# Performance work log

Hardware: AMD Instinct MI355X
Metric: run time of the kernel (lower is better)

Reference implementation:

```python
import jax, jax.numpy as jnp
import numpy as np

P = 16            # decode steps == n_process
M = 4             # number of physical nodes
CAPACITY = [4, 4, 4, 4]
B = 4096          # batch
S = 16            # n_process (sequence length)
G = 128           # gnn_dim
E = 256           # n_embed
H = 512           # n_hidden
CLIP = 10.0       # clip_logits
MASK_PENALTY = 1e8


def setup_inputs() -> dict:
    key = jax.random.key(0)
    ks = jax.random.split(key, 16)
    u = lambda k, shape: jax.random.uniform(k, shape, jnp.float32, -0.08, 0.08)
    return {
        "x": jax.random.normal(ks[0], (B, S, G), jnp.float32),
        "emb_W": u(ks[1], (E, G)),                 # embedding Linear (no bias)
        "enc_Wih": u(ks[2], (4 * H, E)),           # encoder LSTM (gate order i,f,g,o)
        "enc_Whh": u(ks[3], (4 * H, H)),
        "enc_b": u(ks[4], (4 * H,)),               # b_ih + b_hh folded into one bias
        "dec_Wih": u(ks[5], (4 * H, E)),           # decoder LSTM
        "dec_Whh": u(ks[6], (4 * H, H)),
        "dec_b": u(ks[7], (4 * H,)),
        "Wq2": u(ks[8], (H, H)),                   # pointer W_q2
        "bq2": u(ks[9], (H,)),
        "Wref2": u(ks[10], (H, H)),                # pointer W_ref2 (conv1d k=1 == linear)
        "bref2": u(ks[11], (H,)),
        "Vec2": u(ks[12], (H,)),
        "dec_input0": u(ks[13], (E,)),             # learned initial decoder input
    }


def lstm_cell(x, h, c, Wih, Whh, b):
    g = x @ Wih.T + h @ Whh.T + b
    i, f, gg, o = jnp.split(g, 4, axis=-1)
    c = jax.nn.sigmoid(f) * c + jax.nn.sigmoid(i) * jnp.tanh(gg)
    h = jax.nn.sigmoid(o) * jnp.tanh(c)
    return h, c


def reference(x, emb_W, enc_Wih, enc_Whh, enc_b, dec_Wih, dec_Whh, dec_b,
              Wq2, bq2, Wref2, bref2, Vec2, dec_input0):
    Bx, Sx, _ = x.shape
    emb = x @ emb_W.T                                  # (B,S,E)

    # ---- encoder LSTM over the sequence ----
    def enc_step(carry, xt):
        h, c = carry
        h, c = lstm_cell(xt, h, c, enc_Wih, enc_Whh, enc_b)
        return (h, c), h

    h0 = jnp.zeros((Bx, H), emb.dtype)
    (h, c), enc_hs = jax.lax.scan(enc_step, (h0, h0), jnp.swapaxes(emb, 0, 1))
    ref = jnp.swapaxes(enc_hs, 0, 1)                   # (B,S,H)

    # W_ref2 conv1d(k=1) applied to ref is step-invariant: hoist out of the loop
    u2 = jnp.einsum('bsh,oh->bso', ref, Wref2) + bref2  # (B,S,H)

    dec0 = jnp.broadcast_to(dec_input0, (Bx, E))
    mask0 = jnp.zeros((Bx, Sx), emb.dtype)

    def dec_step(carry, _):
        h, c, din, mask = carry
        h, c = lstm_cell(din, h, c, dec_Wih, dec_Whh, dec_b)
        qp = h @ Wq2.T + bq2                           # (B,H)
        t = CLIP * jnp.tanh(qp[:, None, :] + u2)       # (B,S,H)
        logits = jnp.einsum('h,bsh->bs', Vec2, t) - MASK_PENALTY * mask
        log_p = jax.nn.log_softmax(logits, axis=-1)    # (B,S)
        nxt = jnp.argmax(log_p, axis=1)                # greedy node selector
        din = jnp.take_along_axis(emb, nxt[:, None, None], axis=1)[:, 0, :]
        mask = mask + jax.nn.one_hot(nxt, Sx, dtype=mask.dtype)
        return (h, c, din, mask), (nxt, log_p)

    _, (pis, log_ps) = jax.lax.scan(dec_step, (h, c, dec0, mask0), None, length=P)
    pi = jnp.swapaxes(pis, 0, 1)                       # (B,P)
    log_ps = jnp.swapaxes(log_ps, 0, 1)                # (B,P,S)

    # log-likelihood of the chosen tour
    ll = jnp.take_along_axis(log_ps, pi[:, :, None], axis=2)[..., 0].sum(axis=1)

    # __get_mapping: node id per step depends only on the capacity vector
    nodes = jnp.asarray(np.repeat(np.arange(M), np.asarray(CAPACITY))[:P], jnp.int32)
    rows = jnp.arange(Bx)
    mapping = jnp.full((Bx, P), -1, jnp.int32)
    mapping = mapping.at[rows[:, None], pi].set(jnp.broadcast_to(nodes, (Bx, P)))
    return mapping, ll
```

## Files before the change

### kernel.cpp

```cpp
#include <hip/hip_runtime.h>
#include <cstddef>

#define Bsz  4096
#define Sseq 16
#define Gdim 128
#define Edim 256
#define Hdim 512
#define H4   2048
#define Psteps 16
#define BK   16

typedef short bfrag8 __attribute__((ext_vector_type(8)));
typedef float f32x4  __attribute__((ext_vector_type(4)));

__device__ __forceinline__ void split3(float f, unsigned short& h,
                                       unsigned short& m, unsigned short& l) {
    unsigned u = __float_as_uint(f);
    h = (unsigned short)(u >> 16);
    float r1 = f - __uint_as_float(u & 0xffff0000u);
    unsigned u1 = __float_as_uint(r1);
    m = (unsigned short)(u1 >> 16);
    float r2 = r1 - __uint_as_float(u1 & 0xffff0000u);
    l = (unsigned short)(__float_as_uint(r2) >> 16);
}

__global__ void fold_kernel(const float* __restrict__ encWih,
                            const float* __restrict__ encWhh,
                            const float* __restrict__ enc_b,
                            const float* __restrict__ decWih,
                            const float* __restrict__ decWhh,
                            const float* __restrict__ dec_b,
                            const float* __restrict__ embW,
                            const float* __restrict__ dec0,
                            unsigned short* __restrict__ encEh,
                            unsigned short* __restrict__ encEm,
                            unsigned short* __restrict__ encEl,
                            unsigned short* __restrict__ encWh,
                            unsigned short* __restrict__ encWm,
                            unsigned short* __restrict__ encWl,
                            unsigned short* __restrict__ decEh,
                            unsigned short* __restrict__ decEm,
                            unsigned short* __restrict__ decEl,
                            unsigned short* __restrict__ decWh,
                            unsigned short* __restrict__ decWm,
                            unsigned short* __restrict__ decWl,
                            float* __restrict__ encBI, float* __restrict__ decBI,
                            float* __restrict__ v0bI) {
    __shared__ float rE[Edim], rD[Edim];
    const int o = blockIdx.x;
    const int gate = o >> 9, j = o & 511;
    const int c = j * 4 + gate;
    const int g = threadIdx.x;
    rE[g]        = encWih[(size_t)o * Edim + g];
    rE[g + Gdim] = encWih[(size_t)o * Edim + g + Gdim];
    rD[g]        = decWih[(size_t)o * Edim + g];
    rD[g + Gdim] = decWih[(size_t)o * Edim + g + Gdim];
    __syncthreads();

    float se = 0.f, sd = 0.f;
#pragma unroll 8
    for (int e = 0; e < Edim; ++e) {
        float w = embW[e * Gdim + g];
        se += rE[e] * w;
        sd += rD[e] * w;
    }
    unsigned short h, m, l;
    split3(se, h, m, l);
    encEh[(size_t)c * Gdim + g] = h; encEm[(size_t)c * Gdim + g] = m;
    encEl[(size_t)c * Gdim + g] = l;
    split3(sd, h, m, l);
    decEh[(size_t)c * Gdim + g] = h; decEm[(size_t)c * Gdim + g] = m;
    decEl[(size_t)c * Gdim + g] = l;
    for (int k = g; k < Hdim; k += Gdim) {
        split3(encWhh[(size_t)o * Hdim + k], h, m, l);
        encWh[(size_t)c * Hdim + k] = h; encWm[(size_t)c * Hdim + k] = m;
        encWl[(size_t)c * Hdim + k] = l;
        split3(decWhh[(size_t)o * Hdim + k], h, m, l);
        decWh[(size_t)c * Hdim + k] = h; decWm[(size_t)c * Hdim + k] = m;
        decWl[(size_t)c * Hdim + k] = l;
    }
    if (g == 0) {
        encBI[c] = enc_b[o];
        decBI[c] = dec_b[o];
        float s = dec_b[o];
        for (int e = 0; e < Edim; ++e) s += rD[e] * dec0[e];
        v0bI[c] = s;
    }
}

__global__ __launch_bounds__(256) void fold_proj(
    const float* __restrict__ Wr, const float* __restrict__ Wq,
    unsigned short* __restrict__ rWh, unsigned short* __restrict__ rWm,
    unsigned short* __restrict__ rWl,
    unsigned short* __restrict__ qWh, unsigned short* __restrict__ qWm,
    unsigned short* __restrict__ qWl) {
    const int o = blockIdx.x;
    const float* src = blockIdx.y ? Wq : Wr;
    unsigned short* ph = blockIdx.y ? qWh : rWh;
    unsigned short* pm = blockIdx.y ? qWm : rWm;
    unsigned short* pl = blockIdx.y ? qWl : rWl;
    for (int k = threadIdx.x; k < Hdim; k += 256) {
        unsigned short h, m, l;
        split3(src[(size_t)o * Hdim + k], h, m, l);
        ph[(size_t)o * Hdim + k] = h;
        pm[(size_t)o * Hdim + k] = m;
        pl[(size_t)o * Hdim + k] = l;
    }
}

__global__ __launch_bounds__(256) void gates_mfma(
    const unsigned short* __restrict__ Wh1, const unsigned short* __restrict__ Wm1,
    const unsigned short* __restrict__ Wl1, int K1,
    const float* __restrict__ X, int ldx,
    const int* __restrict__ gather, int gmul,
    const unsigned short* __restrict__ Wh2, const unsigned short* __restrict__ Wm2,
    const unsigned short* __restrict__ Wl2, int K2,
    const float* __restrict__ Hin,
    const float* __restrict__ biasI,
    const float* __restrict__ c_in, float* __restrict__ h_out,
    float* __restrict__ c_out, int czero)
{
    __shared__ __align__(16) unsigned short wlds[2][3 * 4096];

    const int tid = threadIdx.x;
    const int wv = tid >> 6, lane = tid & 63;
    const int lm = lane & 15, quad = lane >> 4;
    const int c0 = blockIdx.y * 128;
    const int mB0 = blockIdx.x * 64;

    const int mrow = mB0 + wv * 16 + lm;

    int srow[2], sqs[2];
#pragma unroll
    for (int i = 0; i < 2; ++i) {
        const int seg = i * 4 + wv;
        const int r = seg * 16 + (lane >> 2);
        srow[i] = r;
        sqs[i] = (lane & 3) ^ ((r >> 1) & 3);
    }
    size_t roff1[2], roff2[2];
#pragma unroll
    for (int i = 0; i < 2; ++i) {
        roff1[i] = (size_t)(c0 + srow[i]) * K1 + (size_t)(sqs[i] * 8);
        roff2[i] = (size_t)(c0 + srow[i]) * K2 + (size_t)(sqs[i] * 8);
    }

    const float* xr = nullptr;
    const float* hr = nullptr;
    if (X) {
        size_t off = (size_t)mrow * ldx;
        if (gather) off += (size_t)gather[mrow] * gmul;
        xr = X + off;
    }
    if (Hin) hr = Hin + (size_t)mrow * K2;

    int boffW[8];
#pragma unroll
    for (int tn = 0; tn < 8; ++tn) {
        const int r = tn * 16 + lm;
        boffW[tn] = r * 32 + ((quad ^ ((r >> 1) & 3)) * 8);
    }

    auto stage = [&](int kcN, int buf) {
        const bool nX = kcN < K1;
        const int kb = nX ? kcN : kcN - K1;
#pragma unroll
        for (int i = 0; i < 2; ++i) {
            const int seg = i * 4 + wv;
            unsigned short* lb = &wlds[buf][seg * 512];
            const unsigned short* gh = (nX ? Wh1 + roff1[i] : Wh2 + roff2[i]) + kb;
            const unsigned short* gm = (nX ? Wm1 + roff1[i] : Wm2 + roff2[i]) + kb;
            const unsigned short* gl = (nX ? Wl1 + roff1[i] : Wl2 + roff2[i]) + kb;
            __builtin_amdgcn_global_load_lds(
                (const __attribute__((address_space(1))) void*)gh,
                (__attribute__((address_space(3))) void*)(lb), 16, 0, 0);
            __builtin_amdgcn_global_load_lds(
                (const __attribute__((address_space(1))) void*)gm,
                (__attribute__((address_space(3))) void*)(lb + 4096), 16, 0, 0);
            __builtin_amdgcn_global_load_lds(
                (const __attribute__((address_space(1))) void*)gl,
                (__attribute__((address_space(3))) void*)(lb + 8192), 16, 0, 0);
        }
    };

    f32x4 acc[8];
#pragma unroll
    for (int i = 0; i < 8; ++i) acc[i] = (f32x4){0.f, 0.f, 0.f, 0.f};

    const int KT = K1 + K2;
    stage(0, 0);
    int cur = 0;

    for (int kc = 0; kc < KT; kc += 32) {
        __syncthreads();
        if (kc + 32 < KT) stage(kc + 32, cur ^ 1);

        const bool inX = kc < K1;
        const int kk = (inX ? kc : kc - K1) + quad * 8;

        const float* p = (inX ? xr : hr) + kk;
        float a8[8];
        *(float4*)&a8[0] = *(const float4*)(p);
        *(float4*)&a8[4] = *(const float4*)(p + 4);
        bfrag8 bh, bm, bl;
#pragma unroll
        for (int j = 0; j < 8; ++j) {
            unsigned short h, m, l;
            split3(a8[j], h, m, l);
            bh[j] = (short)h; bm[j] = (short)m; bl[j] = (short)l;
        }

        const unsigned short* bufp = wlds[cur];
#pragma unroll
        for (int hh = 0; hh < 2; ++hh) {
            bfrag8 ah[4], am4[4], al[4];
#pragma unroll
            for (int t = 0; t < 4; ++t) {
                const int tn = hh * 4 + t;
                ah[t]  = *(const bfrag8*)(bufp + boffW[tn]);
                am4[t] = *(const bfrag8*)(bufp + 4096 + boffW[tn]);
                al[t]  = *(const bfrag8*)(bufp + 8192 + boffW[tn]);
            }
#pragma unroll
            for (int t = 0; t < 4; ++t) {
                const int tn = hh * 4 + t;
                f32x4 c = acc[tn];
                c = __builtin_amdgcn_mfma_f32_16x16x32_bf16(ah[t], bl, c, 0, 0, 0);
                c = __builtin_amdgcn_mfma_f32_16x16x32_bf16(al[t], bh, c, 0, 0, 0);
                c = __builtin_amdgcn_mfma_f32_16x16x32_bf16(am4[t], bm, c, 0, 0, 0);
                c = __builtin_amdgcn_mfma_f32_16x16x32_bf16(ah[t], bm, c, 0, 0, 0);
                c = __builtin_amdgcn_mfma_f32_16x16x32_bf16(am4[t], bh, c, 0, 0, 0);
                c = __builtin_amdgcn_mfma_f32_16x16x32_bf16(ah[t], bh, c, 0, 0, 0);
                acc[tn] = c;
            }
        }
        cur ^= 1;
    }

#pragma unroll
    for (int tn = 0; tn < 8; ++tn) {
        const int nb = c0 + tn * 16 + quad * 4;
        float4 bb = *(const float4*)(biasI + nb);
        const int j = nb >> 2;
        const size_t idx = (size_t)mrow * Hdim + j;
        float gi = acc[tn][0] + bb.x;
        float gf = acc[tn][1] + bb.y;
        float gg = acc[tn][2] + bb.z;
        float go = acc[tn][3] + bb.w;
        float si = 1.f / (1.f + expf(-gi));
        float sf = 1.f / (1.f + expf(-gf));
        float so = 1.f / (1.f + expf(-go));
        float co = czero ? 0.f : c_in[idx];
        float cn = si * tanhf(gg) + sf * co;
        c_out[idx] = cn;
        h_out[idx] = so * tanhf(cn);
    }
}

__global__ __launch_bounds__(256) void proj_mfma(
    const unsigned short* __restrict__ Wh, const unsigned short* __restrict__ Wm,
    const unsigned short* __restrict__ Wl,
    const float* __restrict__ A,
    const float* __restrict__ bias,
    float* __restrict__ C, int ldc)
{
    __shared__ __align__(16) unsigned short wlds[2][3 * 2048];
    __shared__ __align__(16) float alds[2][64 * 32];

    const int tid = threadIdx.x;
    const int wv = tid >> 6, lane = tid & 63;
    const int lm = lane & 15, quad = lane >> 4;
    const int nB0 = blockIdx.y * 64;
    const int mB0 = blockIdx.x * 64;

    const int rw = tid >> 2;
    const int sqw = (tid & 3) ^ ((rw >> 1) & 3);
    const size_t wroff = (size_t)(nB0 + rw) * Hdim + (size_t)(sqw * 8);

    const int asw = ((lane & 7) ^ (lane >> 3)) * 4;
    const float* asrc[2];
#pragma unroll
    for (int i = 0; i < 2; ++i) {
        const int r = i * 32 + wv * 8 + (lane >> 3);
        asrc[i] = A + (size_t)(mB0 + r) * Hdim + asw;
    }

    int boffW[4];
#pragma unroll
    for (int tn = 0; tn < 4; ++tn) {
        const int r = tn * 16 + lm;
        boffW[tn] = r * 32 + ((quad ^ ((r >> 1) & 3)) * 8);
    }
    const int ra = wv * 16 + lm;
    const int boffA1 = ra * 32 + (((2 * quad)     ^ (lm & 7)) << 2);
    const int boffA2 = ra * 32 + (((2 * quad + 1) ^ (lm & 7)) << 2);

    auto stage = [&](int kb, int buf) {
        unsigned short* lb0 = &wlds[buf][wv * 512];
        __builtin_amdgcn_global_load_lds(
            (const __attribute__((address_space(1))) void*)(Wh + wroff + kb),
            (__attribute__((address_space(3))) void*)(lb0), 16, 0, 0);
        __builtin_amdgcn_global_load_lds(
            (const __attribute__((address_space(1))) void*)(Wm + wroff + kb),
            (__attribute__((address_space(3))) void*)(lb0 + 2048), 16, 0, 0);
        __builtin_amdgcn_global_load_lds(
            (const __attribute__((address_space(1))) void*)(Wl + wroff + kb),
            (__attribute__((address_space(3))) void*)(lb0 + 4096), 16, 0, 0);
#pragma unroll
        for (int i = 0; i < 2; ++i) {
            float* lb = &alds[buf][(i * 32 + wv * 8) * 32];
            __builtin_amdgcn_global_load_lds(
                (const __attribute__((address_space(1))) void*)(asrc[i] + kb),
                (__attribute__((address_space(3))) void*)lb, 16, 0, 0);
        }
    };

    f32x4 acc[4];
#pragma unroll
    for (int i = 0; i < 4; ++i) acc[i] = (f32x4){0.f, 0.f, 0.f, 0.f};

    stage(0, 0);
    int cur = 0;

    for (int kc = 0; kc < Hdim; kc += 32) {
        __syncthreads();
        if (kc + 32 < Hdim) stage(kc + 32, cur ^ 1);

        const float* abuf = alds[cur];
        float a8[8];
        *(float4*)&a8[0] = *(const float4*)(abuf + boffA1);
        *(float4*)&a8[4] = *(const float4*)(abuf + boffA2);
        bfrag8 bh, bm, bl;
#pragma unroll
        for (int j = 0; j < 8; ++j) {
            unsigned short h, m, l;
            split3(a8[j], h, m, l);
            bh[j] = (short)h; bm[j] = (short)m; bl[j] = (short)l;
        }

        const unsigned short* bufp = wlds[cur];
#pragma unroll
        for (int tn = 0; tn < 4; ++tn) {
            bfrag8 ah  = *(const bfrag8*)(bufp + boffW[tn]);
            bfrag8 am4 = *(const bfrag8*)(bufp + 2048 + boffW[tn]);
            bfrag8 al  = *(const bfrag8*)(bufp + 4096 + boffW[tn]);
            f32x4 c = acc[tn];
            c = __builtin_amdgcn_mfma_f32_16x16x32_bf16(ah,  bl, c, 0, 0, 0);
            c = __builtin_amdgcn_mfma_f32_16x16x32_bf16(al,  bh, c, 0, 0, 0);
            c = __builtin_amdgcn_mfma_f32_16x16x32_bf16(am4, bm, c, 0, 0, 0);
            c = __builtin_amdgcn_mfma_f32_16x16x32_bf16(ah,  bm, c, 0, 0, 0);
            c = __builtin_amdgcn_mfma_f32_16x16x32_bf16(am4, bh, c, 0, 0, 0);
            c = __builtin_amdgcn_mfma_f32_16x16x32_bf16(ah,  bh, c, 0, 0, 0);
            acc[tn] = c;
        }
        cur ^= 1;
    }

    const int m = mB0 + wv * 16 + lm;
#pragma unroll
    for (int tn = 0; tn < 4; ++tn) {
        const int n = nB0 + tn * 16 + quad * 4;
        float4 bb = *(const float4*)(bias + n);
        float4 o;
        o.x = acc[tn][0] + bb.x;
        o.y = acc[tn][1] + bb.y;
        o.z = acc[tn][2] + bb.z;
        o.w = acc[tn][3] + bb.w;
        *(float4*)(C + (size_t)m * ldc + n) = o;
    }
}

__global__ __launch_bounds__(256) void attn_step(const float* __restrict__ qp,
                                                 const float* __restrict__ u2,
                                                 const float* __restrict__ Vec2,
                                                 float* __restrict__ mask,
                                                 float* __restrict__ ll_ws,
                                                 int* __restrict__ nxt,
                                                 float* __restrict__ out_map,
                                                 float* __restrict__ out_ll,
                                                 int step, int node) {
    const int b = blockIdx.x;
    __shared__ float qpS[Hdim];
    __shared__ float vS[Hdim];
    __shared__ float logitS[Sseq];
    const int tid = threadIdx.x;
    qpS[tid]       = qp[(size_t)b * Hdim + tid];
    qpS[tid + 256] = qp[(size_t)b * Hdim + 256 + tid];
    vS[tid]        = Vec2[tid];
    vS[tid + 256]  = Vec2[256 + tid];
    __syncthreads();

    const int wave = tid >> 6, lane = tid & 63;
    for (int si = 0; si < 4; ++si) {
        int s = wave * 4 + si;
        const float* u2p = u2 + ((size_t)b * Sseq + s) * Hdim;
        float sum = 0.f;
#pragma unroll
        for (int i = 0; i < 8; ++i) {
            int hh = lane + i * 64;
            sum += vS[hh] * tanhf(qpS[hh] + u2p[hh]);
        }
        for (int off = 32; off > 0; off >>= 1) sum += __shfl_down(sum, off);
        if (lane == 0) {
            float pen = step ? mask[b * Sseq + s] * 1e8f : 0.f;
            logitS[s] = 10.f * sum - pen;
        }
    }
    __syncthreads();

    if (tid == 0) {
        float mx = logitS[0];
        int am = 0;
        for (int s = 1; s < Sseq; ++s)
            if (logitS[s] > mx) { mx = logitS[s]; am = s; }
        float se = 0.f;
        for (int s = 0; s < Sseq; ++s) se += expf(logitS[s] - mx);
        float lp = -logf(se);
        float llv = (step ? ll_ws[b] : 0.f) + lp;
        ll_ws[b] = llv;
        out_ll[b] = llv;
        nxt[b] = am;
        if (step == 0) {
            for (int s = 0; s < Sseq; ++s) mask[b * Sseq + s] = (s == am) ? 1.f : 0.f;
        } else {
            mask[b * Sseq + am] += 1.f;
        }
        out_map[b * Sseq + am] = (float)node;
    }
}

extern "C" void kernel_launch(void* const* d_in, const int* in_sizes, int n_in,
                              void* d_out, int out_size, void* d_ws, size_t ws_size,
                              hipStream_t stream) {
    const float* x       = (const float*)d_in[0];
    const float* emb_W   = (const float*)d_in[1];
    const float* enc_Wih = (const float*)d_in[2];
    const float* enc_Whh = (const float*)d_in[3];
    const float* enc_b   = (const float*)d_in[4];
    const float* dec_Wih = (const float*)d_in[5];
    const float* dec_Whh = (const float*)d_in[6];
    const float* dec_b   = (const float*)d_in[7];
    const float* Wq2     = (const float*)d_in[8];
    const float* bq2     = (const float*)d_in[9];
    const float* Wref2   = (const float*)d_in[10];
    const float* bref2   = (const float*)d_in[11];
    const float* Vec2    = (const float*)d_in[12];
    const float* dec0    = (const float*)d_in[13];

    float* ws      = (float*)d_ws;
    float* u2      = ws;
    float* h0      = u2 + (size_t)Bsz * Sseq * Hdim;
    float* c0      = h0 + (size_t)Bsz * Hdim;
    float* h1      = c0 + (size_t)Bsz * Hdim;
    float* c1      = h1 + (size_t)Bsz * Hdim;
    float* qp      = c1 + (size_t)Bsz * Hdim;
    float* mask    = qp + (size_t)Bsz * Hdim;
    float* ll      = mask + (size_t)Bsz * Sseq;
    int*   nxt     = (int*)(ll + Bsz);
    float* encBI   = (float*)(nxt + Bsz);
    float* decBI   = encBI + H4;
    float* v0bI    = decBI + H4;
    unsigned short* us = (unsigned short*)(v0bI + H4);
    unsigned short* encEh = us;                       us += (size_t)H4 * Gdim;
    unsigned short* encEm = us;                       us += (size_t)H4 * Gdim;
    unsigned short* encEl = us;                       us += (size_t)H4 * Gdim;
    unsigned short* encWh = us;                       us += (size_t)H4 * Hdim;
    unsigned short* encWm = us;                       us += (size_t)H4 * Hdim;
    unsigned short* encWl = us;                       us += (size_t)H4 * Hdim;
    unsigned short* decEh = us;                       us += (size_t)H4 * Gdim;
    unsigned short* decEm = us;                       us += (size_t)H4 * Gdim;
    unsigned short* decEl = us;                       us += (size_t)H4 * Gdim;
    unsigned short* decWh = us;                       us += (size_t)H4 * Hdim;
    unsigned short* decWm = us;                       us += (size_t)H4 * Hdim;
    unsigned short* decWl = us;                       us += (size_t)H4 * Hdim;
    unsigned short* prWh = us;                        us += (size_t)Hdim * Hdim;
    unsigned short* prWm = us;                        us += (size_t)Hdim * Hdim;
    unsigned short* prWl = us;                        us += (size_t)Hdim * Hdim;
    unsigned short* pqWh = us;                        us += (size_t)Hdim * Hdim;
    unsigned short* pqWm = us;                        us += (size_t)Hdim * Hdim;
    unsigned short* pqWl = us;                        us += (size_t)Hdim * Hdim;

    float* out_map = (float*)d_out;
    float* out_ll  = out_map + (size_t)Bsz * Psteps;

    static const int nodes[Psteps] = {0,0,0,0, 1,1,1,1, 2,2,2,2, 3,3,3,3};

    fold_kernel<<<H4, Gdim, 0, stream>>>(enc_Wih, enc_Whh, enc_b,
                                         dec_Wih, dec_Whh, dec_b,
                                         emb_W, dec0,
                                         encEh, encEm, encEl, encWh, encWm, encWl,
                                         decEh, decEm, decEl, decWh, decWm, decWl,
                                         encBI, decBI, v0bI);
    fold_proj<<<dim3(Hdim, 2), 256, 0, stream>>>(Wref2, Wq2,
                                                 prWh, prWm, prWl,
                                                 pqWh, pqWm, pqWl);

    const dim3 gBig(64, 16);
    const dim3 gPr(64, 8);

    for (int t = 0; t < Sseq; ++t) {
        float* ho = (t & 1) ? h0 : h1;
        float* co = (t & 1) ? c0 : c1;
        const float* hi = (t & 1) ? h1 : h0;
        const float* ci = (t & 1) ? c1 : c0;
        if (t == 0) {
            gates_mfma<<<gBig, 256, 0, stream>>>(
                encEh, encEm, encEl, Gdim,
                x, Sseq * Gdim, nullptr, 0,
                nullptr, nullptr, nullptr, 0, nullptr,
                encBI, ci, ho, co, 1);
        } else {
            gates_mfma<<<gBig, 256, 0, stream>>>(
                encEh, encEm, encEl, Gdim,
                x + t * Gdim, Sseq * Gdim, nullptr, 0,
                encWh, encWm, encWl, Hdim, hi,
                encBI, ci, ho, co, 0);
        }
        proj_mfma<<<gPr, 256, 0, stream>>>(prWh, prWm, prWl, ho, bref2,
                                           u2 + (size_t)t * Hdim, Sseq * Hdim);
    }

    for (int p = 0; p < Psteps; ++p) {
        const int u = Sseq + p;
        float* ho = (u & 1) ? h0 : h1;
        float* co = (u & 1) ? c0 : c1;
        const float* hi = (u & 1) ? h1 : h0;
        const float* ci = (u & 1) ? c1 : c0;
        if (p == 0) {
            gates_mfma<<<gBig, 256, 0, stream>>>(
                nullptr, nullptr, nullptr, 0,
                nullptr, 0, nullptr, 0,
                decWh, decWm, decWl, Hdim, hi,
                v0bI, ci, ho, co, 0);
        } else {
            gates_mfma<<<gBig, 256, 0, stream>>>(
                decEh, decEm, decEl, Gdim,
                x, Sseq * Gdim, nxt, Gdim,
                decWh, decWm, decWl, Hdim, hi,
                decBI, ci, ho, co, 0);
        }
        proj_mfma<<<gPr, 256, 0, stream>>>(pqWh, pqWm, pqWl, ho, bq2,
                                           qp, Hdim);
        attn_step<<<Bsz, 256, 0, stream>>>(qp, u2, Vec2, mask, ll, nxt,
                                           out_map, out_ll, p, nodes[p]);
    }
}
```

Before: 3.836 ms.

## Double batch tile per block and stage activations through LDS with async loads

The gates kernel now uses 512 threads (8 waves) and 128 batch rows per block, halving grid.x so each staged weight tile is reused across twice as many rows. Activation rows (x or h) are no longer read straight from global memory by each lane. They are prefetched into a swizzled, double-buffered LDS array with global_load_lds alongside the weights. This cuts weight traffic and hides activation load latency, at the cost of more LDS per block (about 80KB) and possibly lower occupancy.

After: 3.280 ms. 14.5% less time.

```diff
diff --git a/kernel.cpp b/kernel.cpp
--- a/kernel.cpp
+++ b/kernel.cpp
@@ -108,7 +108,7 @@
     }
 }
 
-__global__ __launch_bounds__(256) void gates_mfma(
+__global__ __launch_bounds__(512) void gates_mfma(
     const unsigned short* __restrict__ Wh1, const unsigned short* __restrict__ Wm1,
     const unsigned short* __restrict__ Wl1, int K1,
     const float* __restrict__ X, int ldx,
@@ -121,38 +121,35 @@
     float* __restrict__ c_out, int czero)
 {
     __shared__ __align__(16) unsigned short wlds[2][3 * 4096];
+    __shared__ __align__(16) float alds[2][128 * 32];
 
     const int tid = threadIdx.x;
     const int wv = tid >> 6, lane = tid & 63;
     const int lm = lane & 15, quad = lane >> 4;
     const int c0 = blockIdx.y * 128;
-    const int mB0 = blockIdx.x * 64;
+    const int mB0 = blockIdx.x * 128;
 
     const int mrow = mB0 + wv * 16 + lm;
 
-    int srow[2], sqs[2];
+    const int srow = wv * 16 + (lane >> 2);
+    const int sqs = (lane & 3) ^ ((srow >> 1) & 3);
+    const size_t roff1 = (size_t)(c0 + srow) * K1 + (size_t)(sqs * 8);
+    const size_t roff2 = (size_t)(c0 + srow) * K2 + (size_t)(sqs * 8);
+
+    const int asw = ((lane & 7) ^ (lane >> 3)) * 4;
+    const float* asrcX[2];
+    const float* asrcH[2];
 #pragma unroll
     for (int i = 0; i < 2; ++i) {
-        const int seg = i * 4 + wv;
-        const int r = seg * 16 + (lane >> 2);
-        srow[i] = r;
-        sqs[i] = (lane & 3) ^ ((r >> 1) & 3);
-    }
-    size_t roff1[2], roff2[2];
-#pragma unroll
-    for (int i = 0; i < 2; ++i) {
-        roff1[i] = (size_t)(c0 + srow[i]) * K1 + (size_t)(sqs[i] * 8);
-        roff2[i] = (size_t)(c0 + srow[i]) * K2 + (size_t)(sqs[i] * 8);
-    }
-
-    const float* xr = nullptr;
-    const float* hr = nullptr;
-    if (X) {
-        size_t off = (size_t)mrow * ldx;
-        if (gather) off += (size_t)gather[mrow] * gmul;
-        xr = X + off;
-    }
-    if (Hin) hr = Hin + (size_t)mrow * K2;
+        const int r = i * 64 + wv * 8 + (lane >> 3);
+        const int m = mB0 + r;
+        if (X) {
+            size_t off = (size_t)m * ldx;
+            if (gather) off += (size_t)gather[m] * gmul;
+            asrcX[i] = X + off + asw;
+        }
+        if (Hin) asrcH[i] = Hin + (size_t)m * K2 + asw;
+    }
 
     int boffW[8];
 #pragma unroll
@@ -160,26 +157,33 @@
         const int r = tn * 16 + lm;
         boffW[tn] = r * 32 + ((quad ^ ((r >> 1) & 3)) * 8);
     }
+    const int ra = wv * 16 + lm;
+    const int boffA1 = ra * 32 + (((2 * quad)     ^ (lm & 7)) << 2);
+    const int boffA2 = ra * 32 + (((2 * quad + 1) ^ (lm & 7)) << 2);
 
     auto stage = [&](int kcN, int buf) {
         const bool nX = kcN < K1;
         const int kb = nX ? kcN : kcN - K1;
+        unsigned short* lb = &wlds[buf][wv * 512];
+        const unsigned short* gh = (nX ? Wh1 + roff1 : Wh2 + roff2) + kb;
+        const unsigned short* gm = (nX ? Wm1 + roff1 : Wm2 + roff2) + kb;
+        const unsigned short* gl = (nX ? Wl1 + roff1 : Wl2 + roff2) + kb;
+        __builtin_amdgcn_global_load_lds(
+            (const __attribute__((address_space(1))) void*)gh,
+            (__attribute__((address_space(3))) void*)(lb), 16, 0, 0);
+        __builtin_amdgcn_global_load_lds(
+            (const __attribute__((address_space(1))) void*)gm,
+            (__attribute__((address_space(3))) void*)(lb + 4096), 16, 0, 0);
+        __builtin_amdgcn_global_load_lds(
+            (const __attribute__((address_space(1))) void*)gl,
+            (__attribute__((address_space(3))) void*)(lb + 8192), 16, 0, 0);
 #pragma unroll
         for (int i = 0; i < 2; ++i) {
-            const int seg = i * 4 + wv;
-            unsigned short* lb = &wlds[buf][seg * 512];
-            const unsigned short* gh = (nX ? Wh1 + roff1[i] : Wh2 + roff2[i]) + kb;
-            const unsigned short* gm = (nX ? Wm1 + roff1[i] : Wm2 + roff2[i]) + kb;
-            const unsigned short* gl = (nX ? Wl1 + roff1[i] : Wl2 + roff2[i]) + kb;
+            float* ab = &alds[buf][(i * 64 + wv * 8) * 32];
+            const float* src = (nX ? asrcX[i] : asrcH[i]) + kb;
             __builtin_amdgcn_global_load_lds(
-                (const __attribute__((address_space(1))) void*)gh,
-                (__attribute__((address_space(3))) void*)(lb), 16, 0, 0);
-            __builtin_amdgcn_global_load_lds(
-                (const __attribute__((address_space(1))) void*)gm,
-                (__attribute__((address_space(3))) void*)(lb + 4096), 16, 0, 0);
-            __builtin_amdgcn_global_load_lds(
-                (const __attribute__((address_space(1))) void*)gl,
-                (__attribute__((address_space(3))) void*)(lb + 8192), 16, 0, 0);
+                (const __attribute__((address_space(1))) void*)src,
+                (__attribute__((address_space(3))) void*)ab, 16, 0, 0);
         }
     };
 
@@ -195,13 +199,10 @@
         __syncthreads();
         if (kc + 32 < KT) stage(kc + 32, cur ^ 1);
 
-        const bool inX = kc < K1;
-        const int kk = (inX ? kc : kc - K1) + quad * 8;
-
-        const float* p = (inX ? xr : hr) + kk;
+        const float* abuf = alds[cur];
         float a8[8];
-        *(float4*)&a8[0] = *(const float4*)(p);
-        *(float4*)&a8[4] = *(const float4*)(p + 4);
+        *(float4*)&a8[0] = *(const float4*)(abuf + boffA1);
+        *(float4*)&a8[4] = *(const float4*)(abuf + boffA2);
         bfrag8 bh, bm, bl;
 #pragma unroll
         for (int j = 0; j < 8; ++j) {
@@ -495,7 +496,7 @@
                                                  prWh, prWm, prWl,
                                                  pqWh, pqWm, pqWl);
 
-    const dim3 gBig(64, 16);
+    const dim3 gBig(32, 16);
     const dim3 gPr(64, 8);
 
     for (int t = 0; t < Sseq; ++t) {
@@ -504,13 +505,13 @@
         const float* hi = (t & 1) ? h1 : h0;
         const float* ci = (t & 1) ? c1 : c0;
         if (t == 0) {
-            gates_mfma<<<gBig, 256, 0, stream>>>(
+            gates_mfma<<<gBig, 512, 0, stream>>>(
                 encEh, encEm, encEl, Gdim,
                 x, Sseq * Gdim, nullptr, 0,
                 nullptr, nullptr, nullptr, 0, nullptr,
                 encBI, ci, ho, co, 1);
         } else {
-            gates_mfma<<<gBig, 256, 0, stream>>>(
+            gates_mfma<<<gBig, 512, 0, stream>>>(
                 encEh, encEm, encEl, Gdim,
                 x + t * Gdim, Sseq * Gdim, nullptr, 0,
                 encWh, encWm, encWl, Hdim, hi,
@@ -527,13 +528,13 @@
         const float* hi = (u & 1) ? h1 : h0;
         const float* ci = (u & 1) ? c1 : c0;
         if (p == 0) {
-            gates_mfma<<<gBig, 256, 0, stream>>>(
+            gates_mfma<<<gBig, 512, 0, stream>>>(
                 nullptr, nullptr, nullptr, 0,
                 nullptr, 0, nullptr, 0,
                 decWh, decWm, decWl, Hdim, hi,
                 v0bI, ci, ho, co, 0);
         } else {
-            gates_mfma<<<gBig, 256, 0, stream>>>(
+            gates_mfma<<<gBig, 512, 0, stream>>>(
                 decEh, decEm, decEl, Gdim,
                 x, Sseq * Gdim, nxt, Gdim,
                 decWh, decWm, decWl, Hdim, hi,
```
